# Performance work log

Hardware: AMD Instinct MI355X
Metric: run time of the kernel (lower is better)

## Reference

```python
import jax, jax.numpy as jnp
import numpy as np

B, L, D_MODEL = 4, 2048, 256
D_STATE, D_CONV, EXPAND = 16, 4, 2
D_INNER = EXPAND * D_MODEL          # 512
DT_RANK = (D_MODEL + 15) // 16      # 16
HORIZON = 96


def setup_inputs() -> dict:
    key = jax.random.key(0)
    ks = jax.random.split(key, 8)
    s = lambda k, shape, scale=0.02: jax.random.normal(k, shape, dtype=jnp.float32) * scale
    return {
        "x": jax.random.normal(ks[0], (B, L, D_MODEL), dtype=jnp.float32),
        "in_proj_w": s(ks[1], (2 * D_INNER, D_MODEL)),          # no bias (mamba default)
        "conv_w": s(ks[2], (D_INNER, 1, D_CONV), 0.1),          # depthwise causal conv
        "conv_b": jnp.zeros((D_INNER,), jnp.float32),
        "x_proj_w": s(ks[3], (DT_RANK + 2 * D_STATE, D_INNER)),
        "dt_proj_w": s(ks[4], (D_INNER, DT_RANK), 0.1),
        # softplus^{-1}(0.01): typical small initial dt
        "dt_proj_b": jnp.log(jnp.expm1(jnp.full((D_INNER,), 0.01, jnp.float32))),
        "A_log": jnp.log(jnp.broadcast_to(jnp.arange(1, D_STATE + 1, dtype=jnp.float32), (D_INNER, D_STATE))),
        "D_param": jnp.ones((D_INNER,), jnp.float32),
        "out_proj_w": s(ks[5], (D_MODEL, D_INNER)),
        "head_w": s(ks[6], (HORIZON, D_MODEL)),
        "head_b": jnp.zeros((HORIZON,), jnp.float32),
    }


def _silu(x):
    return x * jax.nn.sigmoid(x)


def _forward(x, in_proj_w, conv_w, conv_b, x_proj_w, dt_proj_w, dt_proj_b,
             A_log, D_param, out_proj_w, head_w, head_b):
    # in_proj -> split into conv/ssm branch and gate z
    xz = x @ in_proj_w.T                      # (B, L, 2*d_inner)
    x_in, z = jnp.split(xz, 2, axis=-1)
    # depthwise causal conv over time
    x_t = jnp.transpose(x_in, (0, 2, 1))      # (B, d_inner, L)
    x_conv = jax.lax.conv_general_dilated(
        x_t, conv_w, (1,), [(D_CONV - 1, 0)],
        feature_group_count=D_INNER, dimension_numbers=("NCH", "OIH", "NCH"))
    u = _silu(jnp.transpose(x_conv + conv_b[None, :, None], (0, 2, 1)))  # (B, L, d_inner)
    # input-dependent dt, B, C
    x_dbl = u @ x_proj_w.T
    dt, Bm, Cm = jnp.split(x_dbl, [DT_RANK, DT_RANK + D_STATE], axis=-1)
    delta = jax.nn.softplus(dt @ dt_proj_w.T + dt_proj_b)  # (B, L, d_inner)
    A = -jnp.exp(A_log)                                     # (d_inner, d_state)
    deltaA = jnp.exp(delta[..., None] * A)                  # (B, L, d_inner, d_state)
    deltaBu = delta[..., None] * Bm[:, :, None, :] * u[..., None]

    def step(h, ins):
        dA, dBu, c = ins                                    # (B,d,n),(B,d,n),(B,n)
        h = dA * h + dBu
        y = jnp.einsum("bdn,bn->bd", h, c)
        return h, y

    h0 = jnp.zeros((x.shape[0], D_INNER, D_STATE), x.dtype)
    xs = (jnp.moveaxis(deltaA, 1, 0), jnp.moveaxis(deltaBu, 1, 0), jnp.moveaxis(Cm, 1, 0))
    _, ys = jax.lax.scan(step, h0, xs)                      # (L, B, d_inner)
    y = jnp.moveaxis(ys, 0, 1) + u * D_param
    y = y * _silu(z)
    out = y @ out_proj_w.T                                  # (B, L, d_model)
    last = out[:, -1, :]
    return last @ head_w.T + head_b                         # (B, HORIZON)


def reference(x, in_proj_w, conv_w, conv_b, x_proj_w, dt_proj_w, dt_proj_b,
              A_log, D_param, out_proj_w, head_w, head_b):
    return _forward(x, in_proj_w, conv_w, conv_b, x_proj_w, dt_proj_w, dt_proj_b,
                    A_log, D_param, out_proj_w, head_w, head_b)
```

## Files before the change

### kernel.cpp

```cpp
#include <hip/hip_runtime.h>
#include <math.h>

#define BATCH 4
#define LSEQ 2048
#define BL (BATCH*LSEQ)
#define DMODEL 256
#define DINNER 512
#define NSTATE 16
#define DTRANK 16
#define NPROJ 48
#define HORIZ 96
#define NCH 32
#define TCH (LSEQ/NCH)
#define PSTRIDE (BL*NPROJ)

typedef __attribute__((ext_vector_type(8))) short short8b;
typedef __attribute__((ext_vector_type(4))) short short4b;
typedef __attribute__((ext_vector_type(4))) float f32x4;

__device__ __forceinline__ unsigned short f2bf(float f) {
  unsigned u = __float_as_uint(f);
  u += 0x7FFF + ((u >> 16) & 1);
  return (unsigned short)(u >> 16);
}
__device__ __forceinline__ float bf2f(unsigned short h) {
  return __uint_as_float(((unsigned)h) << 16);
}

__global__ __launch_bounds__(512) void k_front(const float* __restrict__ X,
                                               const float* __restrict__ W,
                                               const float* __restrict__ cw,
                                               const float* __restrict__ cb,
                                               const float* __restrict__ xpw,
                                               const float* __restrict__ opw,
                                               const float* __restrict__ hw,
                                               unsigned short* __restrict__ uTb,
                                               float* __restrict__ part,
                                               float* __restrict__ hwf) {
  __shared__ unsigned short sBX[48 * 264];
  __shared__ unsigned short sw2b[48 * 136];
  __shared__ unsigned short u_ldsb[128 * 40];
  const int tid = threadIdx.x;
  const int bx = blockIdx.x;
  if (bx >= 512) {
    const int fid = bx - 512;
    const int k0 = fid * 8;
    float* scratch = (float*)sBX;
    {
      int m = tid >> 1;
      int half = (tid & 1) << 2;
      *(float4*)&scratch[m * 8 + half] =
        *(const float4*)&opw[(size_t)m * DINNER + k0 + half];
    }
    __syncthreads();
    for (int u = tid; u < HORIZ * 8; u += 512) {
      int t = u >> 3, kk = u & 7;
      const float* hr = &hw[(size_t)t * DMODEL];
      float acc = 0.f;
      #pragma unroll 8
      for (int m = 0; m < DMODEL; ++m) acc = fmaf(hr[m], scratch[m*8 + kk], acc);
      hwf[(size_t)t * DINNER + k0 + kk] = acc;
    }
    return;
  }
  const int btc = bx & 255;
  const int jp  = bx >> 8;
  const int bt0 = btc * 32;
  const bool edge0 = ((bt0 & (LSEQ - 1)) == 0);
  const int lane = tid & 63;
  const int w  = tid >> 6;
  const int fl = lane & 15;
  const int fg = lane >> 4;
  for (int u = tid; u < 1536; u += 512) {
    int tok = u >> 5, ko = u & 31;
    int g = bt0 - 16 + tok;
    if (g < 0) g = 0;
    const float* xr = &X[(size_t)g * DMODEL + ko * 8];
    float4 a = *(const float4*)xr, b = *(const float4*)(xr + 4);
    unsigned short t8[8] = {f2bf(a.x), f2bf(a.y), f2bf(a.z), f2bf(a.w),
                            f2bf(b.x), f2bf(b.y), f2bf(b.z), f2bf(b.w)};
    *(short8b*)&sBX[tok * 264 + ko * 8] = *(short8b*)t8;
  }
  const int sj = tid >> 2;
  const int sk = tid & 3;
  const int tf = w & 1;
  const int of = w >> 1;
  f32x4 xacc = {0.f, 0.f, 0.f, 0.f};
  for (int jc = 0; jc < 2; ++jc) {
    const int jbase = jp * 256 + jc * 128;
    __syncthreads();
    for (int u = tid; u < 768; u += 512) {
      int o = u >> 4, k8 = (u & 15) * 8;
      const float* src = &xpw[(size_t)o * DINNER + jbase + k8];
      float4 a = *(const float4*)src, b = *(const float4*)(src + 4);
      unsigned short t8[8] = {f2bf(a.x), f2bf(a.y), f2bf(a.z), f2bf(a.w),
                              f2bf(b.x), f2bf(b.y), f2bf(b.z), f2bf(b.w)};
      *(short8b*)&sw2b[o * 136 + k8] = *(short8b*)t8;
    }
    short8b aw[8];
    {
      const float* wrow = &W[(size_t)(jbase + w * 16 + fl) * DMODEL + fg * 8];
      #pragma unroll
      for (int ks = 0; ks < 8; ++ks) {
        float4 a = *(const float4*)(wrow + ks * 32);
        float4 b = *(const float4*)(wrow + ks * 32 + 4);
        unsigned short t8[8] = {f2bf(a.x), f2bf(a.y), f2bf(a.z), f2bf(a.w),
                                f2bf(b.x), f2bf(b.y), f2bf(b.z), f2bf(b.w)};
        aw[ks] = *(short8b*)t8;
      }
    }
    f32x4 acc0 = {0,0,0,0}, acc1 = {0,0,0,0}, acc2 = {0,0,0,0};
    #pragma unroll
    for (int ks = 0; ks < 8; ++ks) {
      const int kcol = (ks * 4 + fg) * 8;
      short8b x0 = *(short8b*)&sBX[(fl)      * 264 + kcol];
      short8b x1 = *(short8b*)&sBX[(16 + fl) * 264 + kcol];
      short8b x2 = *(short8b*)&sBX[(32 + fl) * 264 + kcol];
      acc0 = __builtin_amdgcn_mfma_f32_16x16x32_bf16(x0, aw[ks], acc0, 0, 0, 0);
      acc1 = __builtin_amdgcn_mfma_f32_16x16x32_bf16(x1, aw[ks], acc1, 0, 0, 0);
      acc2 = __builtin_amdgcn_mfma_f32_16x16x32_bf16(x2, aw[ks], acc2, 0, 0, 0);
    }
    if (edge0) acc0 = (f32x4){0,0,0,0};
    const int j = jbase + w * 16 + fl;
    const float4 cwv = *(const float4*)&cw[j * 4];
    const float cbv = cb[j];
    float u1[4], u2[4];
    {
      float s3a = __shfl(acc1[3], lane - 16), s3b = __shfl(acc0[3], lane + 48);
      float s2a = __shfl(acc1[2], lane - 16), s2b = __shfl(acc0[2], lane + 48);
      float s1a = __shfl(acc1[1], lane - 16), s1b = __shfl(acc0[1], lane + 48);
      float p1 = fg ? s3a : s3b, p2 = fg ? s2a : s2b, p3 = fg ? s1a : s1b;
      float xm1[4] = {p1, acc1[0], acc1[1], acc1[2]};
      float xm2[4] = {p2, p1, acc1[0], acc1[1]};
      float xm3[4] = {p3, p2, p1, acc1[0]};
      #pragma unroll
      for (int r = 0; r < 4; ++r) {
        float s = cbv;
        s = fmaf(cwv.x, xm3[r], s); s = fmaf(cwv.y, xm2[r], s);
        s = fmaf(cwv.z, xm1[r], s); s = fmaf(cwv.w, acc1[r], s);
        u1[r] = s / (1.f + __expf(-s));
      }
    }
    {
      float s3a = __shfl(acc2[3], lane - 16), s3b = __shfl(acc1[3], lane + 48);
      float s2a = __shfl(acc2[2], lane - 16), s2b = __shfl(acc1[2], lane + 48);
      float s1a = __shfl(acc2[1], lane - 16), s1b = __shfl(acc1[1], lane + 48);
      float p1 = fg ? s3a : s3b, p2 = fg ? s2a : s2b, p3 = fg ? s1a : s1b;
      float xm1[4] = {p1, acc2[0], acc2[1], acc2[2]};
      float xm2[4] = {p2, p1, acc2[0], acc2[1]};
      float xm3[4] = {p3, p2, p1, acc2[0]};
      #pragma unroll
      for (int r = 0; r < 4; ++r) {
        float s = cbv;
        s = fmaf(cwv.x, xm3[r], s); s = fmaf(cwv.y, xm2[r], s);
        s = fmaf(cwv.z, xm1[r], s); s = fmaf(cwv.w, acc2[r], s);
        u2[r] = s / (1.f + __expf(-s));
      }
    }
    {
      const int jl = w * 16 + fl;
      unsigned short b1[4] = {f2bf(u1[0]), f2bf(u1[1]), f2bf(u1[2]), f2bf(u1[3])};
      unsigned short b2[4] = {f2bf(u2[0]), f2bf(u2[1]), f2bf(u2[2]), f2bf(u2[3])};
      *(short4b*)&u_ldsb[jl * 40 + fg * 4]      = *(short4b*)b1;
      *(short4b*)&u_ldsb[jl * 40 + 16 + fg * 4] = *(short4b*)b2;
    }
    __syncthreads();
    {
      const int tq = sk * 8;
      *(short8b*)&uTb[(size_t)(jbase + sj) * BL + bt0 + tq] =
        *(short8b*)&u_ldsb[sj * 40 + tq];
    }
    if (w < 6) {
      #pragma unroll
      for (int s = 0; s < 4; ++s) {
        unsigned short ua[8];
        #pragma unroll
        for (int e = 0; e < 8; ++e)
          ua[e] = u_ldsb[(s * 32 + fg * 8 + e) * 40 + tf * 16 + fl];
        short8b wb = *(short8b*)&sw2b[(of * 16 + fl) * 136 + s * 32 + fg * 8];
        xacc = __builtin_amdgcn_mfma_f32_16x16x32_bf16(*(short8b*)ua, wb,
                                                       xacc, 0, 0, 0);
      }
    }
  }
  if (w < 6) {
    float4 v = make_float4(xacc[0], xacc[1], xacc[2], xacc[3]);
    *(float4*)&part[(size_t)jp * PSTRIDE +
                    (size_t)(bt0 + tf * 16 + fl) * NPROJ + of * 16 + fg * 4] = v;
  }
}

__global__ __launch_bounds__(256) void k_scan(const unsigned short* __restrict__ uTb,
                                              const float* __restrict__ part,
                                              const float* __restrict__ dtw,
                                              const float* __restrict__ dtb,
                                              const float* __restrict__ Alog,
                                              float* __restrict__ aprod,
                                              float* __restrict__ hacc) {
  __shared__ float sdt[64][17];
  __shared__ float sB[64][16];
  __shared__ float sdp[16][66][2];
  __shared__ float su[16][68];
  __shared__ float sdtw[16][17];
  __shared__ float sdtb[16];
  const int dblk = blockIdx.x, c = blockIdx.y, b = blockIdx.z;
  const int tid = threadIdx.x;
  const int d0 = dblk * 16;
  const int bt0 = b * LSEQ + c * TCH;
  {
    int tok = tid >> 2, q = (tid & 3) << 2;
    size_t base = (size_t)(bt0 + tok) * NPROJ + q;
    float4 v0 = *(const float4*)&part[base];
    float4 v1 = *(const float4*)&part[base + PSTRIDE];
    sdt[tok][q] = v0.x + v1.x; sdt[tok][q + 1] = v0.y + v1.y;
    sdt[tok][q + 2] = v0.z + v1.z; sdt[tok][q + 3] = v0.w + v1.w;
    float4 w0 = *(const float4*)&part[base + DTRANK];
    float4 w1 = *(const float4*)&part[base + DTRANK + PSTRIDE];
    float4 ww = make_float4(w0.x + w1.x, w0.y + w1.y, w0.z + w1.z, w0.w + w1.w);
    *(float4*)&sB[tok][q] = ww;
    int dl = tid >> 4, t4 = (tid & 15) << 2;
    short4b uv = *(const short4b*)&uTb[(size_t)(d0 + dl) * BL + bt0 + t4];
    su[dl][t4 + 0] = bf2f((unsigned short)uv[0]);
    su[dl][t4 + 1] = bf2f((unsigned short)uv[1]);
    su[dl][t4 + 2] = bf2f((unsigned short)uv[2]);
    su[dl][t4 + 3] = bf2f((unsigned short)uv[3]);
    sdtw[tid >> 4][tid & 15] = dtw[(d0 + (tid >> 4)) * DTRANK + (tid & 15)];
    if (tid < 16) sdtb[tid] = dtb[d0 + tid];
  }
  __syncthreads();
  {
    int tok = tid >> 2, dl4 = (tid & 3) << 2;
    #pragma unroll
    for (int dd = 0; dd < 4; ++dd) {
      int dl = dl4 + dd;
      float a = sdtb[dl];
      #pragma unroll
      for (int r = 0; r < DTRANK; ++r) a = fmaf(sdt[tok][r], sdtw[dl][r], a);
      float dlt = (a > 20.f) ? a : log1pf(__expf(a));
      sdp[dl][tok][0] = dlt;
      sdp[dl][tok][1] = dlt * su[dl][tok];
    }
  }
  __syncthreads();
  const int dl = tid >> 4, n = tid & 15;
  const int d = d0 + dl;
  const float A = -__expf(Alog[d * NSTATE + n]);
  float ap = 1.f, h = 0.f;
  #pragma unroll 8
  for (int tt = 0; tt < TCH; ++tt) {
    float2 dp = *(const float2*)&sdp[dl][tt][0];
    float dA = __expf(dp.x * A);
    h = fmaf(dA, h, dp.y * sB[tt][n]);
    ap *= dA;
  }
  size_t off = (((size_t)b * NCH + c) * DINNER + d) * NSTATE + n;
  aprod[off] = ap;
  hacc[off] = h;
}

__global__ __launch_bounds__(256) void k_combine(const float* __restrict__ aprod,
                                                 const float* __restrict__ hacc,
                                                 const float* __restrict__ part,
                                                 const unsigned short* __restrict__ uTb,
                                                 const float* __restrict__ Dp,
                                                 const float* __restrict__ X,
                                                 const float* __restrict__ ipw,
                                                 float* __restrict__ ybuf) {
  __shared__ float sx[DMODEL];
  const int dblk = blockIdx.x & 31, b = blockIdx.x >> 5;
  const int tid = threadIdx.x;
  const int dl = tid >> 4, n = tid & 15;
  const int d = dblk * 16 + dl;
  sx[tid] = X[((size_t)b * LSEQ + LSEQ - 1) * DMODEL + tid];
  float h = 0.f;
  for (int c = 0; c < NCH; ++c) {
    size_t off = (((size_t)b * NCH + c) * DINNER + d) * NSTATE + n;
    h = fmaf(aprod[off], h, hacc[off]);
  }
  __syncthreads();
  float zp = 0.f;
  {
    const float* zr = &ipw[(size_t)(DINNER + d) * DMODEL + (n << 4)];
    #pragma unroll
    for (int q = 0; q < 4; ++q) {
      float4 w4 = *(const float4*)&zr[q << 2];
      float4 x4 = *(const float4*)&sx[(n << 4) + (q << 2)];
      zp = fmaf(w4.x, x4.x, zp); zp = fmaf(w4.y, x4.y, zp);
      zp = fmaf(w4.z, x4.z, zp); zp = fmaf(w4.w, x4.w, zp);
    }
  }
  const int btL = b * LSEQ + LSEQ - 1;
  size_t cbase = (size_t)btL * NPROJ + DTRANK + NSTATE + n;
  float Cv = part[cbase] + part[cbase + PSTRIDE];
  float v = h * Cv;
  #pragma unroll
  for (int off = 1; off < 16; off <<= 1) {
    v  += __shfl_xor(v, off);
    zp += __shfl_xor(zp, off);
  }
  if (n == 0) {
    float y = v + bf2f(uTb[(size_t)d * BL + btL]) * Dp[d];
    ybuf[b * DINNER + d] = y * zp / (1.f + __expf(-zp));
  }
}

__global__ __launch_bounds__(256) void k_out(const float* __restrict__ sy,
                                             const float* __restrict__ hwf,
                                             const float* __restrict__ hb,
                                             float* __restrict__ out) {
  const int t = blockIdx.x;
  const int b = threadIdx.x >> 6;
  const int lane = threadIdx.x & 63;
  const int k0 = lane << 3;
  const float* yr = &sy[(size_t)b * DINNER + k0];
  const float* wr = &hwf[(size_t)t * DINNER + k0];
  float4 y0 = *(const float4*)yr, y1 = *(const float4*)(yr + 4);
  float4 w0 = *(const float4*)wr, w1 = *(const float4*)(wr + 4);
  float s = y0.x * w0.x + y0.y * w0.y + y0.z * w0.z + y0.w * w0.w
          + y1.x * w1.x + y1.y * w1.y + y1.z * w1.z + y1.w * w1.w;
  #pragma unroll
  for (int off = 1; off < 64; off <<= 1) s += __shfl_xor(s, off);
  if (lane == 0) out[b * HORIZ + t] = s + hb[t];
}

extern "C" void kernel_launch(void* const* d_in, const int* in_sizes, int n_in,
                              void* d_out, int out_size, void* d_ws, size_t ws_size,
                              hipStream_t stream) {
  (void)in_sizes; (void)n_in; (void)out_size; (void)ws_size;
  const float* x    = (const float*)d_in[0];
  const float* ipw  = (const float*)d_in[1];
  const float* cw   = (const float*)d_in[2];
  const float* cb   = (const float*)d_in[3];
  const float* xpw  = (const float*)d_in[4];
  const float* dtw  = (const float*)d_in[5];
  const float* dtb  = (const float*)d_in[6];
  const float* Alog = (const float*)d_in[7];
  const float* Dp   = (const float*)d_in[8];
  const float* opw  = (const float*)d_in[9];
  const float* hw   = (const float*)d_in[10];
  const float* hb   = (const float*)d_in[11];
  float* out = (float*)d_out;
  float* ws  = (float*)d_ws;

  unsigned short* uTb = (unsigned short*)ws;
  float* part  = ws + 2097152;
  float* aprod = ws + 2883584;
  float* hacc  = ws + 3932160;
  float* ybuf  = ws + 4980736;
  float* hwf   = ws + 4982784;

  k_front<<<576, 512, 0, stream>>>(x, ipw, cw, cb, xpw, opw, hw, uTb, part, hwf);
  k_scan<<<dim3(32, NCH, BATCH), 256, 0, stream>>>(uTb, part, dtw, dtb, Alog, aprod, hacc);
  k_combine<<<128, 256, 0, stream>>>(aprod, hacc, part, uTb, Dp, x, ipw, ybuf);
  k_out<<<HORIZ, 256, 0, stream>>>(ybuf, hwf, hb, out);
}
```

Baseline: 72.55 us.

## Split front kernel into four channel groups and store u token-major

The front kernel now assigns 128 inner channels to each block instead of 256, which doubles the block count and drops the inner jc loop. The x_proj partial sums therefore come in four slices instead of two, and the scan and combine kernels add all four. The intermediate u buffer changes from channel-major to token-major, so the LDS transpose and the x_proj MFMA operand reads become contiguous vector loads rather than strided scalar gathers. In exchange, the in_proj activation tile is loaded and converted twice as often, and the partial-sum buffer grows and needs more reads downstream.

```diff
diff --git a/kernel.cpp b/kernel.cpp
--- a/kernel.cpp
+++ b/kernel.cpp
@@ -39,11 +39,11 @@
                                                float* __restrict__ hwf) {
   __shared__ unsigned short sBX[48 * 264];
   __shared__ unsigned short sw2b[48 * 136];
-  __shared__ unsigned short u_ldsb[128 * 40];
+  __shared__ unsigned short u_ldsb[32 * 136];
   const int tid = threadIdx.x;
   const int bx = blockIdx.x;
-  if (bx >= 512) {
-    const int fid = bx - 512;
+  if (bx >= 1024) {
+    const int fid = bx - 1024;
     const int k0 = fid * 8;
     float* scratch = (float*)sBX;
     {
@@ -65,6 +65,7 @@
   }
   const int btc = bx & 255;
   const int jp  = bx >> 8;
+  const int jbase = jp * 128;
   const int bt0 = btc * 32;
   const bool edge0 = ((bt0 & (LSEQ - 1)) == 0);
   const int lane = tid & 63;
@@ -81,109 +82,100 @@
                             f2bf(b.x), f2bf(b.y), f2bf(b.z), f2bf(b.w)};
     *(short8b*)&sBX[tok * 264 + ko * 8] = *(short8b*)t8;
   }
-  const int sj = tid >> 2;
-  const int sk = tid & 3;
+  for (int u = tid; u < 768; u += 512) {
+    int o = u >> 4, k8 = (u & 15) * 8;
+    const float* src = &xpw[(size_t)o * DINNER + jbase + k8];
+    float4 a = *(const float4*)src, b = *(const float4*)(src + 4);
+    unsigned short t8[8] = {f2bf(a.x), f2bf(a.y), f2bf(a.z), f2bf(a.w),
+                            f2bf(b.x), f2bf(b.y), f2bf(b.z), f2bf(b.w)};
+    *(short8b*)&sw2b[o * 136 + k8] = *(short8b*)t8;
+  }
+  short8b aw[8];
+  {
+    const float* wrow = &W[(size_t)(jbase + w * 16 + fl) * DMODEL + fg * 8];
+    #pragma unroll
+    for (int ks = 0; ks < 8; ++ks) {
+      float4 a = *(const float4*)(wrow + ks * 32);
+      float4 b = *(const float4*)(wrow + ks * 32 + 4);
+      unsigned short t8[8] = {f2bf(a.x), f2bf(a.y), f2bf(a.z), f2bf(a.w),
+                              f2bf(b.x), f2bf(b.y), f2bf(b.z), f2bf(b.w)};
+      aw[ks] = *(short8b*)t8;
+    }
+  }
+  __syncthreads();
+  f32x4 acc0 = {0,0,0,0}, acc1 = {0,0,0,0}, acc2 = {0,0,0,0};
+  #pragma unroll
+  for (int ks = 0; ks < 8; ++ks) {
+    const int kcol = (ks * 4 + fg) * 8;
+    short8b x0 = *(short8b*)&sBX[(fl)      * 264 + kcol];
+    short8b x1 = *(short8b*)&sBX[(16 + fl) * 264 + kcol];
+    short8b x2 = *(short8b*)&sBX[(32 + fl) * 264 + kcol];
+    acc0 = __builtin_amdgcn_mfma_f32_16x16x32_bf16(x0, aw[ks], acc0, 0, 0, 0);
+    acc1 = __builtin_amdgcn_mfma_f32_16x16x32_bf16(x1, aw[ks], acc1, 0, 0, 0);
+    acc2 = __builtin_amdgcn_mfma_f32_16x16x32_bf16(x2, aw[ks], acc2, 0, 0, 0);
+  }
+  if (edge0) acc0 = (f32x4){0,0,0,0};
+  const int j = jbase + w * 16 + fl;
+  const float4 cwv = *(const float4*)&cw[j * 4];
+  const float cbv = cb[j];
+  float u1[4], u2[4];
+  {
+    float s3a = __shfl(acc1[3], lane - 16), s3b = __shfl(acc0[3], lane + 48);
+    float s2a = __shfl(acc1[2], lane - 16), s2b = __shfl(acc0[2], lane + 48);
+    float s1a = __shfl(acc1[1], lane - 16), s1b = __shfl(acc0[1], lane + 48);
+    float p1 = fg ? s3a : s3b, p2 = fg ? s2a : s2b, p3 = fg ? s1a : s1b;
+    float xm1[4] = {p1, acc1[0], acc1[1], acc1[2]};
+    float xm2[4] = {p2, p1, acc1[0], acc1[1]};
+    float xm3[4] = {p3, p2, p1, acc1[0]};
+    #pragma unroll
+    for (int r = 0; r < 4; ++r) {
+      float s = cbv;
+      s = fmaf(cwv.x, xm3[r], s); s = fmaf(cwv.y, xm2[r], s);
+      s = fmaf(cwv.z, xm1[r], s); s = fmaf(cwv.w, acc1[r], s);
+      u1[r] = s / (1.f + __expf(-s));
+    }
+  }
+  {
+    float s3a = __shfl(acc2[3], lane - 16), s3b = __shfl(acc1[3], lane + 48);
+    float s2a = __shfl(acc2[2], lane - 16), s2b = __shfl(acc1[2], lane + 48);
+    float s1a = __shfl(acc2[1], lane - 16), s1b = __shfl(acc1[1], lane + 48);
+    float p1 = fg ? s3a : s3b, p2 = fg ? s2a : s2b, p3 = fg ? s1a : s1b;
+    float xm1[4] = {p1, acc2[0], acc2[1], acc2[2]};
+    float xm2[4] = {p2, p1, acc2[0], acc2[1]};
+    float xm3[4] = {p3, p2, p1, acc2[0]};
+    #pragma unroll
+    for (int r = 0; r < 4; ++r) {
+      float s = cbv;
+      s = fmaf(cwv.x, xm3[r], s); s = fmaf(cwv.y, xm2[r], s);
+      s = fmaf(cwv.z, xm1[r], s); s = fmaf(cwv.w, acc2[r], s);
+      u2[r] = s / (1.f + __expf(-s));
+    }
+  }
+  {
+    const int jl = w * 16 + fl;
+    #pragma unroll
+    for (int r = 0; r < 4; ++r) {
+      u_ldsb[(fg * 4 + r) * 136 + jl]        = f2bf(u1[r]);
+      u_ldsb[(16 + fg * 4 + r) * 136 + jl]   = f2bf(u2[r]);
+    }
+  }
+  __syncthreads();
+  {
+    const int tok = tid >> 4;
+    const int j8  = (tid & 15) * 8;
+    *(short8b*)&uTb[(size_t)(bt0 + tok) * DINNER + jbase + j8] =
+      *(short8b*)&u_ldsb[tok * 136 + j8];
+  }
   const int tf = w & 1;
   const int of = w >> 1;
-  f32x4 xacc = {0.f, 0.f, 0.f, 0.f};
-  for (int jc = 0; jc < 2; ++jc) {
-    const int jbase = jp * 256 + jc * 128;
-    __syncthreads();
-    for (int u = tid; u < 768; u += 512) {
-      int o = u >> 4, k8 = (u & 15) * 8;
-      const float* src = &xpw[(size_t)o * DINNER + jbase + k8];
-      float4 a = *(const float4*)src, b = *(const float4*)(src + 4);
-      unsigned short t8[8] = {f2bf(a.x), f2bf(a.y), f2bf(a.z), f2bf(a.w),
-                              f2bf(b.x), f2bf(b.y), f2bf(b.z), f2bf(b.w)};
-      *(short8b*)&sw2b[o * 136 + k8] = *(short8b*)t8;
-    }
-    short8b aw[8];
-    {
-      const float* wrow = &W[(size_t)(jbase + w * 16 + fl) * DMODEL + fg * 8];
-      #pragma unroll
-      for (int ks = 0; ks < 8; ++ks) {
-        float4 a = *(const float4*)(wrow + ks * 32);
-        float4 b = *(const float4*)(wrow + ks * 32 + 4);
-        unsigned short t8[8] = {f2bf(a.x), f2bf(a.y), f2bf(a.z), f2bf(a.w),
-                                f2bf(b.x), f2bf(b.y), f2bf(b.z), f2bf(b.w)};
-        aw[ks] = *(short8b*)t8;
-      }
-    }
-    f32x4 acc0 = {0,0,0,0}, acc1 = {0,0,0,0}, acc2 = {0,0,0,0};
-    #pragma unroll
-    for (int ks = 0; ks < 8; ++ks) {
-      const int kcol = (ks * 4 + fg) * 8;
-      short8b x0 = *(short8b*)&sBX[(fl)      * 264 + kcol];
-      short8b x1 = *(short8b*)&sBX[(16 + fl) * 264 + kcol];
-      short8b x2 = *(short8b*)&sBX[(32 + fl) * 264 + kcol];
-      acc0 = __builtin_amdgcn_mfma_f32_16x16x32_bf16(x0, aw[ks], acc0, 0, 0, 0);
-      acc1 = __builtin_amdgcn_mfma_f32_16x16x32_bf16(x1, aw[ks], acc1, 0, 0, 0);
-      acc2 = __builtin_amdgcn_mfma_f32_16x16x32_bf16(x2, aw[ks], acc2, 0, 0, 0);
-    }
-    if (edge0) acc0 = (f32x4){0,0,0,0};
-    const int j = jbase + w * 16 + fl;
-    const float4 cwv = *(const float4*)&cw[j * 4];
-    const float cbv = cb[j];
-    float u1[4], u2[4];
-    {
-      float s3a = __shfl(acc1[3], lane - 16), s3b = __shfl(acc0[3], lane + 48);
-      float s2a = __shfl(acc1[2], lane - 16), s2b = __shfl(acc0[2], lane + 48);
-      float s1a = __shfl(acc1[1], lane - 16), s1b = __shfl(acc0[1], lane + 48);
-      float p1 = fg ? s3a : s3b, p2 = fg ? s2a : s2b, p3 = fg ? s1a : s1b;
-      float xm1[4] = {p1, acc1[0], acc1[1], acc1[2]};
-      float xm2[4] = {p2, p1, acc1[0], acc1[1]};
-      float xm3[4] = {p3, p2, p1, acc1[0]};
-      #pragma unroll
-      for (int r = 0; r < 4; ++r) {
-        float s = cbv;
-        s = fmaf(cwv.x, xm3[r], s); s = fmaf(cwv.y, xm2[r], s);
-        s = fmaf(cwv.z, xm1[r], s); s = fmaf(cwv.w, acc1[r], s);
-        u1[r] = s / (1.f + __expf(-s));
-      }
-    }
-    {
-      float s3a = __shfl(acc2[3], lane - 16), s3b = __shfl(acc1[3], lane + 48);
-      float s2a = __shfl(acc2[2], lane - 16), s2b = __shfl(acc1[2], lane + 48);
-      float s1a = __shfl(acc2[1], lane - 16), s1b = __shfl(acc1[1], lane + 48);
-      float p1 = fg ? s3a : s3b, p2 = fg ? s2a : s2b, p3 = fg ? s1a : s1b;
-      float xm1[4] = {p1, acc2[0], acc2[1], acc2[2]};
-      float xm2[4] = {p2, p1, acc2[0], acc2[1]};
-      float xm3[4] = {p3, p2, p1, acc2[0]};
-      #pragma unroll
-      for (int r = 0; r < 4; ++r) {
-        float s = cbv;
-        s = fmaf(cwv.x, xm3[r], s); s = fmaf(cwv.y, xm2[r], s);
-        s = fmaf(cwv.z, xm1[r], s); s = fmaf(cwv.w, acc2[r], s);
-        u2[r] = s / (1.f + __expf(-s));
-      }
-    }
-    {
-      const int jl = w * 16 + fl;
-      unsigned short b1[4] = {f2bf(u1[0]), f2bf(u1[1]), f2bf(u1[2]), f2bf(u1[3])};
-      unsigned short b2[4] = {f2bf(u2[0]), f2bf(u2[1]), f2bf(u2[2]), f2bf(u2[3])};
-      *(short4b*)&u_ldsb[jl * 40 + fg * 4]      = *(short4b*)b1;
-      *(short4b*)&u_ldsb[jl * 40 + 16 + fg * 4] = *(short4b*)b2;
-    }
-    __syncthreads();
-    {
-      const int tq = sk * 8;
-      *(short8b*)&uTb[(size_t)(jbase + sj) * BL + bt0 + tq] =
-        *(short8b*)&u_ldsb[sj * 40 + tq];
-    }
-    if (w < 6) {
-      #pragma unroll
-      for (int s = 0; s < 4; ++s) {
-        unsigned short ua[8];
-        #pragma unroll
-        for (int e = 0; e < 8; ++e)
-          ua[e] = u_ldsb[(s * 32 + fg * 8 + e) * 40 + tf * 16 + fl];
-        short8b wb = *(short8b*)&sw2b[(of * 16 + fl) * 136 + s * 32 + fg * 8];
-        xacc = __builtin_amdgcn_mfma_f32_16x16x32_bf16(*(short8b*)ua, wb,
-                                                       xacc, 0, 0, 0);
-      }
-    }
-  }
   if (w < 6) {
+    f32x4 xacc = {0.f, 0.f, 0.f, 0.f};
+    #pragma unroll
+    for (int s = 0; s < 4; ++s) {
+      short8b ua = *(short8b*)&u_ldsb[(tf * 16 + fl) * 136 + s * 32 + fg * 8];
+      short8b wb = *(short8b*)&sw2b[(of * 16 + fl) * 136 + s * 32 + fg * 8];
+      xacc = __builtin_amdgcn_mfma_f32_16x16x32_bf16(ua, wb, xacc, 0, 0, 0);
+    }
     float4 v = make_float4(xacc[0], xacc[1], xacc[2], xacc[3]);
     *(float4*)&part[(size_t)jp * PSTRIDE +
                     (size_t)(bt0 + tf * 16 + fl) * NPROJ + of * 16 + fg * 4] = v;
@@ -200,7 +192,7 @@
   __shared__ float sdt[64][17];
   __shared__ float sB[64][16];
   __shared__ float sdp[16][66][2];
-  __shared__ float su[16][68];
+  __shared__ float su2[64][20];
   __shared__ float sdtw[16][17];
   __shared__ float sdtb[16];
   const int dblk = blockIdx.x, c = blockIdx.y, b = blockIdx.z;
@@ -212,18 +204,25 @@
     size_t base = (size_t)(bt0 + tok) * NPROJ + q;
     float4 v0 = *(const float4*)&part[base];
     float4 v1 = *(const float4*)&part[base + PSTRIDE];
-    sdt[tok][q] = v0.x + v1.x; sdt[tok][q + 1] = v0.y + v1.y;
-    sdt[tok][q + 2] = v0.z + v1.z; sdt[tok][q + 3] = v0.w + v1.w;
+    float4 v2 = *(const float4*)&part[base + 2 * (size_t)PSTRIDE];
+    float4 v3 = *(const float4*)&part[base + 3 * (size_t)PSTRIDE];
+    sdt[tok][q]     = v0.x + v1.x + v2.x + v3.x;
+    sdt[tok][q + 1] = v0.y + v1.y + v2.y + v3.y;
+    sdt[tok][q + 2] = v0.z + v1.z + v2.z + v3.z;
+    sdt[tok][q + 3] = v0.w + v1.w + v2.w + v3.w;
     float4 w0 = *(const float4*)&part[base + DTRANK];
     float4 w1 = *(const float4*)&part[base + DTRANK + PSTRIDE];
-    float4 ww = make_float4(w0.x + w1.x, w0.y + w1.y, w0.z + w1.z, w0.w + w1.w);
+    float4 w2 = *(const float4*)&part[base + DTRANK + 2 * (size_t)PSTRIDE];
+    float4 w3 = *(const float4*)&part[base + DTRANK + 3 * (size_t)PSTRIDE];
+    float4 ww = make_float4(w0.x + w1.x + w2.x + w3.x, w0.y + w1.y + w2.y + w3.y,
+                            w0.z + w1.z + w2.z + w3.z, w0.w + w1.w + w2.w + w3.w);
     *(float4*)&sB[tok][q] = ww;
-    int dl = tid >> 4, t4 = (tid & 15) << 2;
-    short4b uv = *(const short4b*)&uTb[(size_t)(d0 + dl) * BL + bt0 + t4];
-    su[dl][t4 + 0] = bf2f((unsigned short)uv[0]);
-    su[dl][t4 + 1] = bf2f((unsigned short)uv[1]);
-    su[dl][t4 + 2] = bf2f((unsigned short)uv[2]);
-    su[dl][t4 + 3] = bf2f((unsigned short)uv[3]);
+    int d4 = (tid & 3) << 2;
+    short4b uv = *(const short4b*)&uTb[(size_t)(bt0 + tok) * DINNER + d0 + d4];
+    su2[tok][d4 + 0] = bf2f((unsigned short)uv[0]);
+    su2[tok][d4 + 1] = bf2f((unsigned short)uv[1]);
+    su2[tok][d4 + 2] = bf2f((unsigned short)uv[2]);
+    su2[tok][d4 + 3] = bf2f((unsigned short)uv[3]);
     sdtw[tid >> 4][tid & 15] = dtw[(d0 + (tid >> 4)) * DTRANK + (tid & 15)];
     if (tid < 16) sdtb[tid] = dtb[d0 + tid];
   }
@@ -238,7 +237,7 @@
       for (int r = 0; r < DTRANK; ++r) a = fmaf(sdt[tok][r], sdtw[dl][r], a);
       float dlt = (a > 20.f) ? a : log1pf(__expf(a));
       sdp[dl][tok][0] = dlt;
-      sdp[dl][tok][1] = dlt * su[dl][tok];
+      sdp[dl][tok][1] = dlt * su2[tok][dl];
     }
   }
   __syncthreads();
@@ -291,7 +290,8 @@
   }
   const int btL = b * LSEQ + LSEQ - 1;
   size_t cbase = (size_t)btL * NPROJ + DTRANK + NSTATE + n;
-  float Cv = part[cbase] + part[cbase + PSTRIDE];
+  float Cv = part[cbase] + part[cbase + PSTRIDE]
+           + part[cbase + 2 * (size_t)PSTRIDE] + part[cbase + 3 * (size_t)PSTRIDE];
   float v = h * Cv;
   #pragma unroll
   for (int off = 1; off < 16; off <<= 1) {
@@ -299,7 +299,7 @@
     zp += __shfl_xor(zp, off);
   }
   if (n == 0) {
-    float y = v + bf2f(uTb[(size_t)d * BL + btL]) * Dp[d];
+    float y = v + bf2f(uTb[(size_t)btL * DINNER + d]) * Dp[d];
     ybuf[b * DINNER + d] = y * zp / (1.f + __expf(-zp));
   }
 }
@@ -344,12 +344,12 @@
 
   unsigned short* uTb = (unsigned short*)ws;
   float* part  = ws + 2097152;
-  float* aprod = ws + 2883584;
-  float* hacc  = ws + 3932160;
-  float* ybuf  = ws + 4980736;
-  float* hwf   = ws + 4982784;
-
-  k_front<<<576, 512, 0, stream>>>(x, ipw, cw, cb, xpw, opw, hw, uTb, part, hwf);
+  float* aprod = ws + 3670016;
+  float* hacc  = ws + 4718592;
+  float* ybuf  = ws + 5767168;
+  float* hwf   = ws + 5769216;
+
+  k_front<<<1088, 512, 0, stream>>>(x, ipw, cw, cb, xpw, opw, hw, uTb, part, hwf);
   k_scan<<<dim3(32, NCH, BATCH), 256, 0, stream>>>(uTb, part, dtw, dtb, Alog, aprod, hacc);
   k_combine<<<128, 256, 0, stream>>>(aprod, hacc, part, uTb, Dp, x, ipw, ybuf);
   k_out<<<HORIZ, 256, 0, stream>>>(ybuf, hwf, hb, out);
```

Result: slower. 75.46 us (+4.0%).

## Cut scan chunks to 8, move z-gate into front kernel, fuse combine and head

Applied to the files above, without the earlier changes.

The chunked scan drops from 32 chunks of 64 tokens to 8 chunks of 256 tokens, each processed as four 64-token stages. This shrinks the aprod/hacc intermediates and the serial combine work. The z-gate projection for the last token now runs in 8 extra blocks of the front kernel, and the combine and output-head kernels are merged into one 1024-thread kernel per batch, saving a launch. The trade-off is fewer scan blocks (1024 instead of 4096) with a longer serial loop each, which lowers parallelism in the scan.

```diff
diff --git a/kernel.cpp b/kernel.cpp
--- a/kernel.cpp
+++ b/kernel.cpp
@@ -10,8 +10,7 @@
 #define DTRANK 16
 #define NPROJ 48
 #define HORIZ 96
-#define NCH 32
-#define TCH (LSEQ/NCH)
+#define SCH 8
 #define PSTRIDE (BL*NPROJ)
 
 typedef __attribute__((ext_vector_type(8))) short short8b;
@@ -36,13 +35,37 @@
                                                const float* __restrict__ hw,
                                                unsigned short* __restrict__ uTb,
                                                float* __restrict__ part,
-                                               float* __restrict__ hwf) {
+                                               float* __restrict__ hwf,
+                                               float* __restrict__ zbuf) {
   __shared__ unsigned short sBX[48 * 264];
   __shared__ unsigned short sw2b[48 * 136];
   __shared__ unsigned short u_ldsb[128 * 40];
   const int tid = threadIdx.x;
   const int bx = blockIdx.x;
   if (bx >= 512) {
+    if (bx >= 576) {
+      const int fid = bx - 576;
+      const int zb = fid >> 1, dh = fid & 1;
+      float* sx = (float*)sBX;
+      if (tid < 64)
+        *(float4*)&sx[tid * 4] =
+          *(const float4*)&X[((size_t)zb * LSEQ + LSEQ - 1) * DMODEL + tid * 4];
+      __syncthreads();
+      const int d = dh * 256 + (tid >> 1);
+      const int kh = (tid & 1) * 128;
+      const float* zr = &W[(size_t)(DINNER + d) * DMODEL + kh];
+      float zp = 0.f;
+      #pragma unroll 8
+      for (int q = 0; q < 128; q += 4) {
+        float4 w4 = *(const float4*)&zr[q];
+        float4 x4 = *(const float4*)&sx[kh + q];
+        zp = fmaf(w4.x, x4.x, zp); zp = fmaf(w4.y, x4.y, zp);
+        zp = fmaf(w4.z, x4.z, zp); zp = fmaf(w4.w, x4.w, zp);
+      }
+      zp += __shfl_xor(zp, 1);
+      if ((tid & 1) == 0) zbuf[zb * DINNER + d] = zp;
+      return;
+    }
     const int fid = bx - 512;
     const int k0 = fid * 8;
     float* scratch = (float*)sBX;
@@ -206,121 +229,115 @@
   const int dblk = blockIdx.x, c = blockIdx.y, b = blockIdx.z;
   const int tid = threadIdx.x;
   const int d0 = dblk * 16;
-  const int bt0 = b * LSEQ + c * TCH;
-  {
-    int tok = tid >> 2, q = (tid & 3) << 2;
-    size_t base = (size_t)(bt0 + tok) * NPROJ + q;
-    float4 v0 = *(const float4*)&part[base];
-    float4 v1 = *(const float4*)&part[base + PSTRIDE];
-    sdt[tok][q] = v0.x + v1.x; sdt[tok][q + 1] = v0.y + v1.y;
-    sdt[tok][q + 2] = v0.z + v1.z; sdt[tok][q + 3] = v0.w + v1.w;
-    float4 w0 = *(const float4*)&part[base + DTRANK];
-    float4 w1 = *(const float4*)&part[base + DTRANK + PSTRIDE];
-    float4 ww = make_float4(w0.x + w1.x, w0.y + w1.y, w0.z + w1.z, w0.w + w1.w);
-    *(float4*)&sB[tok][q] = ww;
-    int dl = tid >> 4, t4 = (tid & 15) << 2;
-    short4b uv = *(const short4b*)&uTb[(size_t)(d0 + dl) * BL + bt0 + t4];
-    su[dl][t4 + 0] = bf2f((unsigned short)uv[0]);
-    su[dl][t4 + 1] = bf2f((unsigned short)uv[1]);
-    su[dl][t4 + 2] = bf2f((unsigned short)uv[2]);
-    su[dl][t4 + 3] = bf2f((unsigned short)uv[3]);
-    sdtw[tid >> 4][tid & 15] = dtw[(d0 + (tid >> 4)) * DTRANK + (tid & 15)];
-    if (tid < 16) sdtb[tid] = dtb[d0 + tid];
-  }
-  __syncthreads();
-  {
-    int tok = tid >> 2, dl4 = (tid & 3) << 2;
-    #pragma unroll
-    for (int dd = 0; dd < 4; ++dd) {
-      int dl = dl4 + dd;
-      float a = sdtb[dl];
-      #pragma unroll
-      for (int r = 0; r < DTRANK; ++r) a = fmaf(sdt[tok][r], sdtw[dl][r], a);
-      float dlt = (a > 20.f) ? a : log1pf(__expf(a));
-      sdp[dl][tok][0] = dlt;
-      sdp[dl][tok][1] = dlt * su[dl][tok];
-    }
-  }
-  __syncthreads();
+  const int bt0c = b * LSEQ + c * 256;
   const int dl = tid >> 4, n = tid & 15;
   const int d = d0 + dl;
   const float A = -__expf(Alog[d * NSTATE + n]);
   float ap = 1.f, h = 0.f;
-  #pragma unroll 8
-  for (int tt = 0; tt < TCH; ++tt) {
-    float2 dp = *(const float2*)&sdp[dl][tt][0];
-    float dA = __expf(dp.x * A);
-    h = fmaf(dA, h, dp.y * sB[tt][n]);
-    ap *= dA;
-  }
-  size_t off = (((size_t)b * NCH + c) * DINNER + d) * NSTATE + n;
+  for (int st = 0; st < 4; ++st) {
+    const int bt0 = bt0c + st * 64;
+    __syncthreads();
+    {
+      int tok = tid >> 2, q = (tid & 3) << 2;
+      size_t base = (size_t)(bt0 + tok) * NPROJ + q;
+      float4 v0 = *(const float4*)&part[base];
+      float4 v1 = *(const float4*)&part[base + PSTRIDE];
+      sdt[tok][q] = v0.x + v1.x; sdt[tok][q + 1] = v0.y + v1.y;
+      sdt[tok][q + 2] = v0.z + v1.z; sdt[tok][q + 3] = v0.w + v1.w;
+      float4 w0 = *(const float4*)&part[base + DTRANK];
+      float4 w1 = *(const float4*)&part[base + DTRANK + PSTRIDE];
+      float4 ww = make_float4(w0.x + w1.x, w0.y + w1.y, w0.z + w1.z, w0.w + w1.w);
+      *(float4*)&sB[tok][q] = ww;
+      int t4 = (tid & 15) << 2;
+      short4b uv = *(const short4b*)&uTb[(size_t)(d0 + dl) * BL + bt0 + t4];
+      su[dl][t4 + 0] = bf2f((unsigned short)uv[0]);
+      su[dl][t4 + 1] = bf2f((unsigned short)uv[1]);
+      su[dl][t4 + 2] = bf2f((unsigned short)uv[2]);
+      su[dl][t4 + 3] = bf2f((unsigned short)uv[3]);
+      sdtw[tid >> 4][tid & 15] = dtw[(d0 + (tid >> 4)) * DTRANK + (tid & 15)];
+      if (tid < 16) sdtb[tid] = dtb[d0 + tid];
+    }
+    __syncthreads();
+    {
+      int tok = tid >> 2, dl4 = (tid & 3) << 2;
+      #pragma unroll
+      for (int dd = 0; dd < 4; ++dd) {
+        int ddl = dl4 + dd;
+        float a = sdtb[ddl];
+        #pragma unroll
+        for (int r = 0; r < DTRANK; ++r) a = fmaf(sdt[tok][r], sdtw[ddl][r], a);
+        float dlt = (a > 20.f) ? a : log1pf(__expf(a));
+        sdp[ddl][tok][0] = dlt;
+        sdp[ddl][tok][1] = dlt * su[ddl][tok];
+      }
+    }
+    __syncthreads();
+    #pragma unroll 8
+    for (int tt = 0; tt < 64; ++tt) {
+      float2 dp = *(const float2*)&sdp[dl][tt][0];
+      float dA = __expf(dp.x * A);
+      h = fmaf(dA, h, dp.y * sB[tt][n]);
+      ap *= dA;
+    }
+  }
+  size_t off = (((size_t)b * SCH + c) * DINNER + d) * NSTATE + n;
   aprod[off] = ap;
   hacc[off] = h;
 }
 
-__global__ __launch_bounds__(256) void k_combine(const float* __restrict__ aprod,
-                                                 const float* __restrict__ hacc,
-                                                 const float* __restrict__ part,
-                                                 const unsigned short* __restrict__ uTb,
-                                                 const float* __restrict__ Dp,
-                                                 const float* __restrict__ X,
-                                                 const float* __restrict__ ipw,
-                                                 float* __restrict__ ybuf) {
-  __shared__ float sx[DMODEL];
-  const int dblk = blockIdx.x & 31, b = blockIdx.x >> 5;
-  const int tid = threadIdx.x;
-  const int dl = tid >> 4, n = tid & 15;
-  const int d = dblk * 16 + dl;
-  sx[tid] = X[((size_t)b * LSEQ + LSEQ - 1) * DMODEL + tid];
-  float h = 0.f;
-  for (int c = 0; c < NCH; ++c) {
-    size_t off = (((size_t)b * NCH + c) * DINNER + d) * NSTATE + n;
-    h = fmaf(aprod[off], h, hacc[off]);
+__global__ __launch_bounds__(1024) void k_tail(const float* __restrict__ aprod,
+                                               const float* __restrict__ hacc,
+                                               const float* __restrict__ part,
+                                               const unsigned short* __restrict__ uTb,
+                                               const float* __restrict__ Dp,
+                                               const float* __restrict__ zbuf,
+                                               const float* __restrict__ hwf,
+                                               const float* __restrict__ hb,
+                                               float* __restrict__ out) {
+  __shared__ float sy[DINNER];
+  const int b = blockIdx.x;
+  const int t = threadIdx.x;
+  const int d = t >> 1;
+  const int ng = (t & 1) << 3;
+  float h0=0,h1=0,h2=0,h3=0,h4=0,h5=0,h6=0,h7=0;
+  for (int c = 0; c < SCH; ++c) {
+    size_t off = (((size_t)b * SCH + c) * DINNER + d) * NSTATE + ng;
+    float4 a0 = *(const float4*)&aprod[off], a1 = *(const float4*)&aprod[off + 4];
+    float4 g0 = *(const float4*)&hacc[off],  g1 = *(const float4*)&hacc[off + 4];
+    h0 = fmaf(a0.x, h0, g0.x); h1 = fmaf(a0.y, h1, g0.y);
+    h2 = fmaf(a0.z, h2, g0.z); h3 = fmaf(a0.w, h3, g0.w);
+    h4 = fmaf(a1.x, h4, g1.x); h5 = fmaf(a1.y, h5, g1.y);
+    h6 = fmaf(a1.z, h6, g1.z); h7 = fmaf(a1.w, h7, g1.w);
+  }
+  const int btL = b * LSEQ + LSEQ - 1;
+  size_t cbase = (size_t)btL * NPROJ + DTRANK + NSTATE + ng;
+  float4 c0 = *(const float4*)&part[cbase];
+  float4 c1 = *(const float4*)&part[cbase + 4];
+  float4 e0 = *(const float4*)&part[cbase + PSTRIDE];
+  float4 e1 = *(const float4*)&part[cbase + PSTRIDE + 4];
+  float v = h0*(c0.x+e0.x) + h1*(c0.y+e0.y) + h2*(c0.z+e0.z) + h3*(c0.w+e0.w)
+          + h4*(c1.x+e1.x) + h5*(c1.y+e1.y) + h6*(c1.z+e1.z) + h7*(c1.w+e1.w);
+  v += __shfl_xor(v, 1);
+  if ((t & 1) == 0) {
+    float u = bf2f(uTb[(size_t)d * BL + btL]);
+    float z = zbuf[b * DINNER + d];
+    sy[d] = (v + u * Dp[d]) * z / (1.f + __expf(-z));
   }
   __syncthreads();
-  float zp = 0.f;
-  {
-    const float* zr = &ipw[(size_t)(DINNER + d) * DMODEL + (n << 4)];
+  const int wv = t >> 6, lane = t & 63;
+  #pragma unroll
+  for (int q = 0; q < 6; ++q) {
+    const int tt = wv + (q << 4);
+    const float* wr = &hwf[(size_t)tt * DINNER + lane * 8];
+    const float* yr = &sy[lane * 8];
+    float4 w0 = *(const float4*)wr, w1 = *(const float4*)(wr + 4);
+    float4 y0 = *(const float4*)yr, y1 = *(const float4*)(yr + 4);
+    float s = y0.x*w0.x + y0.y*w0.y + y0.z*w0.z + y0.w*w0.w
+            + y1.x*w1.x + y1.y*w1.y + y1.z*w1.z + y1.w*w1.w;
     #pragma unroll
-    for (int q = 0; q < 4; ++q) {
-      float4 w4 = *(const float4*)&zr[q << 2];
-      float4 x4 = *(const float4*)&sx[(n << 4) + (q << 2)];
-      zp = fmaf(w4.x, x4.x, zp); zp = fmaf(w4.y, x4.y, zp);
-      zp = fmaf(w4.z, x4.z, zp); zp = fmaf(w4.w, x4.w, zp);
-    }
-  }
-  const int btL = b * LSEQ + LSEQ - 1;
-  size_t cbase = (size_t)btL * NPROJ + DTRANK + NSTATE + n;
-  float Cv = part[cbase] + part[cbase + PSTRIDE];
-  float v = h * Cv;
-  #pragma unroll
-  for (int off = 1; off < 16; off <<= 1) {
-    v  += __shfl_xor(v, off);
-    zp += __shfl_xor(zp, off);
-  }
-  if (n == 0) {
-    float y = v + bf2f(uTb[(size_t)d * BL + btL]) * Dp[d];
-    ybuf[b * DINNER + d] = y * zp / (1.f + __expf(-zp));
-  }
-}
-
-__global__ __launch_bounds__(256) void k_out(const float* __restrict__ sy,
-                                             const float* __restrict__ hwf,
-                                             const float* __restrict__ hb,
-                                             float* __restrict__ out) {
-  const int t = blockIdx.x;
-  const int b = threadIdx.x >> 6;
-  const int lane = threadIdx.x & 63;
-  const int k0 = lane << 3;
-  const float* yr = &sy[(size_t)b * DINNER + k0];
-  const float* wr = &hwf[(size_t)t * DINNER + k0];
-  float4 y0 = *(const float4*)yr, y1 = *(const float4*)(yr + 4);
-  float4 w0 = *(const float4*)wr, w1 = *(const float4*)(wr + 4);
-  float s = y0.x * w0.x + y0.y * w0.y + y0.z * w0.z + y0.w * w0.w
-          + y1.x * w1.x + y1.y * w1.y + y1.z * w1.z + y1.w * w1.w;
-  #pragma unroll
-  for (int off = 1; off < 64; off <<= 1) s += __shfl_xor(s, off);
-  if (lane == 0) out[b * HORIZ + t] = s + hb[t];
+    for (int off = 1; off < 64; off <<= 1) s += __shfl_xor(s, off);
+    if (lane == 0) out[b * HORIZ + tt] = s + hb[tt];
+  }
 }
 
 extern "C" void kernel_launch(void* const* d_in, const int* in_sizes, int n_in,
@@ -345,12 +362,11 @@
   unsigned short* uTb = (unsigned short*)ws;
   float* part  = ws + 2097152;
   float* aprod = ws + 2883584;
-  float* hacc  = ws + 3932160;
-  float* ybuf  = ws + 4980736;
-  float* hwf   = ws + 4982784;
-
-  k_front<<<576, 512, 0, stream>>>(x, ipw, cw, cb, xpw, opw, hw, uTb, part, hwf);
-  k_scan<<<dim3(32, NCH, BATCH), 256, 0, stream>>>(uTb, part, dtw, dtb, Alog, aprod, hacc);
-  k_combine<<<128, 256, 0, stream>>>(aprod, hacc, part, uTb, Dp, x, ipw, ybuf);
-  k_out<<<HORIZ, 256, 0, stream>>>(ybuf, hwf, hb, out);
-}
+  float* hacc  = ws + 3145728;
+  float* zbuf  = ws + 3407872;
+  float* hwf   = ws + 3409920;
+
+  k_front<<<584, 512, 0, stream>>>(x, ipw, cw, cb, xpw, opw, hw, uTb, part, hwf, zbuf);
+  k_scan<<<dim3(32, SCH, BATCH), 256, 0, stream>>>(uTb, part, dtw, dtb, Alog, aprod, hacc);
+  k_tail<<<BATCH, 1024, 0, stream>>>(aprod, hacc, part, uTb, Dp, zbuf, hwf, hb, out);
+}
```

Measured after the change: 87.51 us. 20.6% more time.
